# Kernel optimization log

Hardware: AMD Instinct MI355X
Metric: run time of the kernel (lower is better)

## Reference

```python
import jax, jax.numpy as jnp
import numpy as np

B, S, HID = 1, 2048, 2048
H, KV, D = 16, 4, 128  # head_dim = HID // H; GQA group size g = H // KV
THETA = 10000.0


def setup_inputs() -> dict:
    key = jax.random.key(0)
    ks = jax.random.split(key, 5)
    s = 0.02  # initializer_range
    return {
        "hidden_states": jax.random.normal(ks[0], (B, S, HID), jnp.float32),
        "wq": jax.random.normal(ks[1], (HID, H * D), jnp.float32) * s,
        "wk": jax.random.normal(ks[2], (HID, KV * D), jnp.float32) * s,
        "wv": jax.random.normal(ks[3], (HID, KV * D), jnp.float32) * s,
        "wo": jax.random.normal(ks[4], (H * D, HID), jnp.float32) * s,
        "attention_mask": jnp.ones((B, S), jnp.int32),
        "position_ids": jnp.broadcast_to(jnp.arange(S, dtype=jnp.int32), (B, S)),
    }


def _rope(x, position_ids):
    # x: [b, s, h, d]; rotate consecutive (even, odd) pairs by angle t * theta^{-2j/d}
    half = D // 2
    inv_freq = 1.0 / (THETA ** (jnp.arange(0, D, 2, dtype=jnp.float32) / D))  # [half]
    ang = position_ids[..., None].astype(jnp.float32) * inv_freq  # [b, s, half]
    cos = jnp.cos(ang)[:, :, None, :]  # [b, s, 1, half]
    sin = jnp.sin(ang)[:, :, None, :]
    xr = x.astype(jnp.float32).reshape(*x.shape[:-1], half, 2)
    x0, x1 = xr[..., 0], xr[..., 1]
    out = jnp.stack((x0 * cos - x1 * sin, x0 * sin + x1 * cos), axis=-1)
    return out.reshape(x.shape)


def reference(hidden_states, wq, wk, wv, wo, attention_mask, position_ids):
    b, s, _ = hidden_states.shape
    g = H // KV
    xq = (hidden_states @ wq).reshape(b, s, H, D)
    xk = (hidden_states @ wk).reshape(b, s, KV, D)
    xv = (hidden_states @ wv).reshape(b, s, KV, D)
    # GQA: each kv head repeated g consecutive times -> H heads (matches einops '(h g)')
    xk = jnp.repeat(xk, g, axis=2)
    xv = jnp.repeat(xv, g, axis=2)
    xq = _rope(xq, position_ids)
    xk = _rope(xk, position_ids)
    # causal + padding mask -> additive bias (0 or -inf), softmax in fp32
    causal = jnp.tril(jnp.ones((s, s), dtype=bool))[None, None]  # [1,1,q,k]
    mask = causal & (attention_mask[:, None, None, :] > 0)  # [b,1,q,k]
    scores = jnp.einsum('bqhd,bkhd->bhqk', xq.astype(jnp.float32), xk.astype(jnp.float32))
    scores = scores / jnp.sqrt(jnp.float32(D))
    scores = jnp.where(mask, scores, jnp.finfo(jnp.float32).min)
    attn_weights = jax.nn.softmax(scores, axis=-1)  # [b,h,q,k] fp32
    attn = jnp.einsum('bhqk,bkhd->bqhd', attn_weights, xv.astype(jnp.float32))
    return (attn.reshape(b, s, H * D).astype(hidden_states.dtype)) @ wo
```

## Files before the change

### kernel.cpp

```cpp
#include <hip/hip_runtime.h>
#include <hip/hip_bf16.h>

#define S_LEN 2048
#define HIDDIM 2048
#define NH 16
#define NKV 4
#define HD 128
#define KVROW 1024
#define QKVN 3072

typedef __attribute__((ext_vector_type(8))) short short8;
typedef __attribute__((ext_vector_type(8))) unsigned short ushort8;
typedef __attribute__((ext_vector_type(4))) unsigned short ushort4v;
typedef __attribute__((ext_vector_type(4))) float f32x4;

__device__ __forceinline__ unsigned short f2bf(float f) {
  union { float f; unsigned int u; } v; v.f = f;
  unsigned int r = (v.u + 0x7FFFu + ((v.u >> 16) & 1u)) >> 16;
  return (unsigned short)r;
}
__device__ __forceinline__ float bf2f(unsigned short h) {
  union { unsigned int u; float f; } v; v.u = ((unsigned int)h) << 16;
  return v.f;
}

__device__ __forceinline__ void gl2lds16(const unsigned short* src,
                                         unsigned short* dst) {
  __builtin_amdgcn_global_load_lds(
      (const __attribute__((address_space(1))) unsigned int*)src,
      (__attribute__((address_space(3))) unsigned int*)dst, 16, 0, 0);
}

__global__ __launch_bounds__(256) void h2b_kernel(const float* __restrict__ H,
                                                  unsigned short* __restrict__ Hb) {
  int i = (blockIdx.x * 256 + threadIdx.x) * 8;
  float4 a = *(const float4*)(H + i), b = *(const float4*)(H + i + 4);
  ushort8 r;
  r[0] = f2bf(a.x); r[1] = f2bf(a.y); r[2] = f2bf(a.z); r[3] = f2bf(a.w);
  r[4] = f2bf(b.x); r[5] = f2bf(b.y); r[6] = f2bf(b.z); r[7] = f2bf(b.w);
  *(ushort8*)(Hb + i) = r;
}

__global__ __launch_bounds__(256) void transpose_w(
    const float* __restrict__ W, unsigned short* __restrict__ Wt,
    int Nsrc, int Kdst, int n_off) {
  __shared__ unsigned short Ts[64][72];
  const int n0 = blockIdx.x * 64, k0 = blockIdx.y * 64;
  const int tid = threadIdx.x;
  const int c2 = (tid & 31) * 2, rb = tid >> 5;
#pragma unroll
  for (int p = 0; p < 8; ++p) {
    int r = rb + p * 8;
    float2 v = *(const float2*)&W[(size_t)(k0 + r) * Nsrc + n0 + c2];
    Ts[c2][r] = f2bf(v.x);
    Ts[c2 + 1][r] = f2bf(v.y);
  }
  __syncthreads();
  const int n = tid >> 2, kq = (tid & 3) * 16;
  ushort8 w0 = *(const ushort8*)&Ts[n][kq];
  ushort8 w1 = *(const ushort8*)&Ts[n][kq + 8];
  size_t base = (size_t)(n_off + n0 + n) * Kdst + k0 + kq;
  *(ushort8*)&Wt[base] = w0;
  *(ushort8*)&Wt[base + 8] = w1;
}

__global__ __launch_bounds__(256) void transpose_v(
    const unsigned short* __restrict__ KVb, unsigned short* __restrict__ Vt) {
  __shared__ unsigned short Ts[64][72];
  const int c0 = blockIdx.x * 64, s0 = blockIdx.y * 64;
  const int tid = threadIdx.x;
  const int sr = tid >> 2, cq = (tid & 3) * 16;
  ushort8 a = *(const ushort8*)&KVb[(size_t)(s0 + sr) * KVROW + 512 + c0 + cq];
  ushort8 b = *(const ushort8*)&KVb[(size_t)(s0 + sr) * KVROW + 512 + c0 + cq + 8];
#pragma unroll
  for (int j = 0; j < 8; ++j) { Ts[cq + j][sr] = a[j]; Ts[cq + 8 + j][sr] = b[j]; }
  __syncthreads();
  const int c = tid >> 2, sq = (tid & 3) * 16;
  ushort8 w0 = *(const ushort8*)&Ts[c][sq];
  ushort8 w1 = *(const ushort8*)&Ts[c][sq + 8];
  *(ushort8*)&Vt[(size_t)(c0 + c) * S_LEN + s0 + sq] = w0;
  *(ushort8*)&Vt[(size_t)(c0 + c) * S_LEN + s0 + sq + 8] = w1;
}

template <bool CF>
__global__ __launch_bounds__(256) void gemm_tn(
    const unsigned short* __restrict__ A, const unsigned short* __restrict__ Bt,
    void* __restrict__ C1, void* __restrict__ C2,
    int M, int N, int K, int splitcol, int ld1, int ld2) {
  __shared__ unsigned short As[128][72];
  __shared__ unsigned short Bs[64][72];
  const int m0 = blockIdx.y * 128, n0 = blockIdx.x * 64;
  const int tid = threadIdx.x, wid = tid >> 6, lane = tid & 63;
  const int wr = wid >> 1, wc = wid & 1;
  const int lr = lane & 15, lg = lane >> 4;

  f32x4 acc[4][2];
#pragma unroll
  for (int m = 0; m < 4; ++m)
#pragma unroll
    for (int n = 0; n < 2; ++n) acc[m][n] = (f32x4){0.f, 0.f, 0.f, 0.f};

  const int ar = tid >> 1, ac = (tid & 1) * 32;
  const int br = tid >> 2, bc = (tid & 3) * 16;

  ushort8 areg[4], breg[2];
  auto loadA = [&](int k0) {
#pragma unroll
    for (int i = 0; i < 4; ++i)
      areg[i] = *(const ushort8*)(A + (size_t)(m0 + ar) * K + k0 + ac + i * 8);
  };
  auto loadB = [&](int k0) {
    breg[0] = *(const ushort8*)(Bt + (size_t)(n0 + br) * K + k0 + bc);
    breg[1] = *(const ushort8*)(Bt + (size_t)(n0 + br) * K + k0 + bc + 8);
  };
  auto writeS = [&]() {
#pragma unroll
    for (int i = 0; i < 4; ++i) *(ushort8*)&As[ar][ac + i * 8] = areg[i];
    *(ushort8*)&Bs[br][bc] = breg[0];
    *(ushort8*)&Bs[br][bc + 8] = breg[1];
  };

  loadA(0); loadB(0);
  writeS();

  for (int k0 = 0; k0 < K; k0 += 64) {
    __syncthreads();
    if (k0 + 64 < K) {
      loadA(k0 + 64); loadB(k0 + 64);
      asm volatile("" ::: "memory");
    }
#pragma unroll
    for (int s = 0; s < 2; ++s) {
      short8 af[4], bfv[2];
#pragma unroll
      for (int m = 0; m < 4; ++m)
        af[m] = *(const short8*)&As[wr * 64 + m * 16 + lr][s * 32 + lg * 8];
#pragma unroll
      for (int n = 0; n < 2; ++n)
        bfv[n] = *(const short8*)&Bs[wc * 32 + n * 16 + lr][s * 32 + lg * 8];
#pragma unroll
      for (int m = 0; m < 4; ++m)
#pragma unroll
        for (int n = 0; n < 2; ++n)
          acc[m][n] = __builtin_amdgcn_mfma_f32_16x16x32_bf16(af[m], bfv[n], acc[m][n], 0, 0, 0);
    }
    __syncthreads();
    if (k0 + 64 < K) writeS();
  }

#pragma unroll
  for (int m = 0; m < 4; ++m)
#pragma unroll
    for (int n = 0; n < 2; ++n)
#pragma unroll
      for (int r = 0; r < 4; ++r) {
        int row = m0 + wr * 64 + m * 16 + lg * 4 + r;
        int col = n0 + wc * 32 + n * 16 + lr;
        float v = acc[m][n][r];
        if (CF) ((float*)C1)[(size_t)row * ld1 + col] = v;
        else if (col < splitcol) ((unsigned short*)C1)[(size_t)row * ld1 + col] = f2bf(v);
        else ((unsigned short*)C2)[(size_t)row * ld2 + (col - splitcol)] = f2bf(v);
      }
}

__global__ void rope2(unsigned short* __restrict__ Q,
                      unsigned short* __restrict__ KV,
                      const int* __restrict__ pos) {
  int idx = blockIdx.x * blockDim.x + threadIdx.x;
  if (idx >= S_LEN * 64) return;
  int s = idx >> 6, j = idx & 63;
  float inv = exp2f(-0.2076205059304703f * (float)j);
  float ang = (float)pos[s] * inv;
  float sn, cs;
  __sincosf(ang, &sn, &cs);
  auto rot = [&](unsigned short* base) {
    unsigned* p = (unsigned*)base;
    unsigned v = *p;
    float x0 = bf2f((unsigned short)(v & 0xffff));
    float x1 = bf2f((unsigned short)(v >> 16));
    unsigned r = (unsigned)f2bf(x0 * cs - x1 * sn) |
                 ((unsigned)f2bf(x0 * sn + x1 * cs) << 16);
    *p = r;
  };
#pragma unroll
  for (int hh = 0; hh < NH; ++hh) rot(Q + (size_t)s * HIDDIM + hh * HD + 2 * j);
#pragma unroll
  for (int hh = 0; hh < NKV; ++hh) rot(KV + (size_t)s * KVROW + hh * HD + 2 * j);
}

__global__ void maskbits_kernel(const int* __restrict__ amask,
                                unsigned* __restrict__ mb) {
  int w = threadIdx.x;
  unsigned m = 0;
#pragma unroll
  for (int b = 0; b < 32; ++b) m |= (amask[w * 32 + b] != 0 ? 1u : 0u) << b;
  mb[w] = m;
}

__global__ __launch_bounds__(512) void attn_kernel(
    const unsigned short* __restrict__ Qb, const unsigned short* __restrict__ KVb,
    const unsigned short* __restrict__ VtG, const unsigned* __restrict__ mbits,
    unsigned short* __restrict__ Ob,
    unsigned short* __restrict__ Opart, float* __restrict__ Lpart, int nsplit) {
  const int x = (int)blockIdx.x;
  const int qt = 63 - (x >> 2);
  const int c = x & 3;
  const int kvh = (int)blockIdx.y;
  const int nch = (qt >> 4) + 1;
  if (nsplit == 0) { if (c != 0) return; }
  else if (c >= nch) return;
  const int qb = qt * 32;
  int kbeg = 0, kend = qb + 32;
  bool partial = false;
  if (nsplit && nch > 1) {
    kbeg = c * 512;
    kend = min(kend, kbeg + 512);
    partial = true;
  }

  __shared__ unsigned short Klds[2][32 * 128];
  __shared__ unsigned short Vlds[2][128 * 32];
  __shared__ unsigned short Plds[8][16][40];
  const int tid = threadIdx.x, wid = tid >> 6, lane = tid & 63;
  const int lr = lane & 15, lg = lane >> 4;
  const int h = kvh * 4 + (wid & 3);
  const int rg = wid >> 2;
  const int qrow0 = qb + rg * 16;

  short8 qf[4];
  {
    const unsigned short* qp = Qb + (size_t)(qrow0 + lr) * HIDDIM + h * HD;
#pragma unroll
    for (int cc = 0; cc < 4; ++cc) qf[cc] = *(const short8*)(qp + cc * 32 + lg * 8);
  }
  f32x4 o[8];
#pragma unroll
  for (int cc = 0; cc < 8; ++cc) o[cc] = (f32x4){0.f, 0.f, 0.f, 0.f};
  float lsum = 0.f;

  const unsigned short* Vg = VtG + (size_t)(kvh * HD) * S_LEN;

  const int ksrow = (wid << 2) + (lane >> 4);
  const int kssrc = ((lane & 15) << 4) ^ ((ksrow & 7) << 4);
  const int vsd = (wid << 4) + (lane >> 2);
  const int vssrc = (((lane & 3) << 4) ^ ((vsd & 3) << 4));

  auto stage = [&](int kt, int b) {
    gl2lds16(KVb + (size_t)(kt + ksrow) * KVROW + kvh * HD + (kssrc >> 1),
             &Klds[b][0] + (size_t)wid * 512);
    gl2lds16(Vg + (size_t)vsd * S_LEN + kt + (vssrc >> 1),
             &Vlds[b][0] + (size_t)wid * 512);
  };

  stage(kbeg, 0);

  const int qr = qrow0 + lr;
  const float SCALE = 0.08838834764831845f;
  int cur = 0;

  for (int kt = kbeg; kt < kend; kt += 32) {
    __syncthreads();
    if (kt + 32 < kend) stage(kt + 32, cur ^ 1);

    f32x4 sc[2];
    sc[0] = (f32x4){0.f, 0.f, 0.f, 0.f};
    sc[1] = (f32x4){0.f, 0.f, 0.f, 0.f};
    const unsigned short* kbase = &Klds[cur][0];
    __builtin_amdgcn_s_setprio(1);
#pragma unroll
    for (int t = 0; t < 2; ++t)
#pragma unroll
      for (int cc = 0; cc < 4; ++cc) {
        short8 kf = *(const short8*)(kbase + ((t * 16 + lr) << 7) +
                                     ((((cc << 6) + (lg << 4)) ^ ((lr & 7) << 4)) >> 1));
        sc[t] = __builtin_amdgcn_mfma_f32_16x16x32_bf16(kf, qf[cc], sc[t], 0, 0, 0);
      }
    __builtin_amdgcn_s_setprio(0);
    const unsigned mw = mbits[kt >> 5];
    float p[2][4];
#pragma unroll
    for (int t = 0; t < 2; ++t)
#pragma unroll
      for (int r = 0; r < 4; ++r) {
        int kk = t * 16 + lg * 4 + r;
        bool ok = (kt + kk <= qr) && ((mw >> kk) & 1u);
        float s = ok ? sc[t][r] * SCALE - 3.0f : -1e30f;
        float pv = __expf(s);
        p[t][r] = pv;
        lsum += pv;
      }
#pragma unroll
    for (int t = 0; t < 2; ++t) {
      ushort4v pk;
#pragma unroll
      for (int r = 0; r < 4; ++r) pk[r] = f2bf(p[t][r]);
      *(ushort4v*)&Plds[wid][lr][t * 16 + lg * 4] = pk;
    }
    short8 pf = *(const short8*)&Plds[wid][lr][lg * 8];
    const unsigned short* vbase = &Vlds[cur][0];
    __builtin_amdgcn_s_setprio(1);
#pragma unroll
    for (int cc = 0; cc < 8; ++cc) {
      short8 vf = *(const short8*)(vbase + ((cc * 16 + lr) << 5) +
                                   ((lg ^ (lr & 3)) << 3));
      o[cc] = __builtin_amdgcn_mfma_f32_16x16x32_bf16(pf, vf, o[cc], 0, 0, 0);
    }
    __builtin_amdgcn_s_setprio(0);
    cur ^= 1;
  }

  float ls = lsum;
  ls += __shfl_xor(ls, 16, 64);
  ls += __shfl_xor(ls, 32, 64);

  if (!partial) {
    float lrec[4];
#pragma unroll
    for (int r = 0; r < 4; ++r) lrec[r] = 1.0f / __shfl(ls, lg * 4 + r, 16);
#pragma unroll
    for (int cc = 0; cc < 8; ++cc)
#pragma unroll
      for (int r = 0; r < 4; ++r) {
        const int row = qrow0 + lg * 4 + r;
        Ob[(size_t)row * HIDDIM + h * HD + cc * 16 + lr] = f2bf(o[cc][r] * lrec[r]);
      }
  } else {
    const int g = qt >> 4, j = qt & 15;
    const int base = (g == 1) ? 0 : (g == 2) ? 32 : 80;
    const int slot = base + j * nch + c + 144 * kvh;
    if (lg == 0) Lpart[slot * 128 + (wid & 3) * 32 + rg * 16 + lr] = ls;
#pragma unroll
    for (int cc = 0; cc < 8; ++cc)
#pragma unroll
      for (int r = 0; r < 4; ++r)
        Opart[(size_t)slot * 16384 + (wid & 3) * 4096 +
              (rg * 16 + lg * 4 + r) * 128 + cc * 16 + lr] = f2bf(o[cc][r]);
  }
}

__global__ __launch_bounds__(256) void combine_kernel(
    const unsigned short* __restrict__ Opart, const float* __restrict__ Lpart,
    unsigned short* __restrict__ Ab) {
  const int qt = 16 + (int)blockIdx.x;
  const int kvh = (int)blockIdx.y;
  const int nch = (qt >> 4) + 1;
  const int g = qt >> 4, j = qt & 15;
  const int base = (g == 1) ? 0 : (g == 2) ? 32 : 80;
  const int s0 = base + j * nch + 144 * kvh;
  const int tid = threadIdx.x;
  const int rowid = tid >> 1;
  const int d0 = (tid & 1) * 64;
  float L = 0.f;
  for (int cc = 0; cc < nch; ++cc) L += Lpart[(s0 + cc) * 128 + rowid];
  const float linv = 1.0f / L;
  const int h = kvh * 4 + (rowid >> 5);
  const int row = qt * 32 + (rowid & 31);
  unsigned short* dst = Ab + (size_t)row * HIDDIM + h * HD + d0;
  for (int i = 0; i < 64; i += 8) {
    float acc[8] = {0, 0, 0, 0, 0, 0, 0, 0};
    for (int cc = 0; cc < nch; ++cc) {
      ushort8 v = *(const ushort8*)&Opart[(size_t)(s0 + cc) * 16384 +
                                          rowid * 128 + d0 + i];
#pragma unroll
      for (int k = 0; k < 8; ++k) acc[k] += bf2f(v[k]);
    }
    ushort8 r;
#pragma unroll
    for (int k = 0; k < 8; ++k) r[k] = f2bf(acc[k] * linv);
    *(ushort8*)(dst + i) = r;
  }
}

extern "C" void kernel_launch(void* const* d_in, const int* in_sizes, int n_in,
                              void* d_out, int out_size, void* d_ws, size_t ws_size,
                              hipStream_t stream) {
  const float* hidden = (const float*)d_in[0];
  const float* wq = (const float*)d_in[1];
  const float* wk = (const float*)d_in[2];
  const float* wv = (const float*)d_in[3];
  const float* wo = (const float*)d_in[4];
  const int* amask = (const int*)d_in[5];
  const int* pos = (const int*)d_in[6];

  unsigned short* Qb = (unsigned short*)d_ws;
  unsigned short* KVb = Qb + (size_t)S_LEN * HIDDIM;
  unsigned short* Ab = KVb + (size_t)S_LEN * KVROW;
  unsigned short* WT1 = Ab + (size_t)S_LEN * HIDDIM;
  unsigned short* Hb = WT1 + (size_t)QKVN * HIDDIM;
  float* out = (float*)d_out;

  unsigned short* Opart = WT1;
  unsigned short* Vt_chunk = WT1 + (size_t)576 * 16384;
  unsigned* mbits_chunk = (unsigned*)((char*)d_ws + 41943040ull);
  float* Lpart = (float*)((char*)d_ws + 41943296ull);
  const size_t need_chunk = 42238208ull;
  unsigned short* Vt_fb = WT1 + (size_t)HIDDIM * HIDDIM;
  unsigned* mbits_fb = (unsigned*)((char*)d_ws + 31457280ull);

  const int nsplit = (ws_size >= need_chunk) ? 1 : 0;
  unsigned short* Vt = nsplit ? Vt_chunk : Vt_fb;
  unsigned* mbits = nsplit ? mbits_chunk : mbits_fb;

  dim3 blk(256);
  h2b_kernel<<<2048, blk, 0, stream>>>(hidden, Hb);
  transpose_w<<<dim3(32, 32), blk, 0, stream>>>(wq, WT1, HIDDIM, HIDDIM, 0);
  transpose_w<<<dim3(8, 32), blk, 0, stream>>>(wk, WT1, 512, HIDDIM, 2048);
  transpose_w<<<dim3(8, 32), blk, 0, stream>>>(wv, WT1, 512, HIDDIM, 2560);
  gemm_tn<false><<<dim3(QKVN / 64, S_LEN / 128), blk, 0, stream>>>(
      Hb, WT1, Qb, KVb, S_LEN, QKVN, HIDDIM, 2048, HIDDIM, KVROW);
  transpose_v<<<dim3(8, 32), blk, 0, stream>>>(KVb, Vt);
  rope2<<<(S_LEN * 64 + 255) / 256, blk, 0, stream>>>(Qb, KVb, pos);
  maskbits_kernel<<<1, 64, 0, stream>>>(amask, mbits);
  attn_kernel<<<dim3(256, NKV), dim3(512), 0, stream>>>(
      Qb, KVb, Vt, mbits, Ab, Opart, Lpart, nsplit);
  if (nsplit)
    combine_kernel<<<dim3(48, NKV), blk, 0, stream>>>(Opart, Lpart, Ab);
  transpose_w<<<dim3(32, 32), blk, 0, stream>>>(wo, WT1, HIDDIM, HIDDIM, 0);
  gemm_tn<true><<<dim3(HIDDIM / 64, S_LEN / 128), blk, 0, stream>>>(
      Ab, WT1, out, nullptr, S_LEN, HIDDIM, HIDDIM, HIDDIM, HIDDIM, 0);
}
```

Before: 184.6 us.

## Stage GEMM tiles via direct global-to-LDS loads with double buffering and XOR swizzle

Replaces the register-staged global→LDS copy in gemm_tn with direct global-to-LDS 16-byte loads (gl2lds16) into double-buffered shared tiles. The padded layout is replaced by an XOR swizzle on 16-byte chunks to avoid LDS bank conflicts. The second barrier per k-step is removed. The aim is to cut VGPR pressure and load/store instruction overhead and to overlap the next tile's fetch with the MFMAs. It doubles LDS use and relies on the async load completing before the single barrier, with no explicit vmcnt wait shown.

```diff
diff --git a/kernel.cpp b/kernel.cpp
--- a/kernel.cpp
+++ b/kernel.cpp
@@ -87,8 +87,8 @@
     const unsigned short* __restrict__ A, const unsigned short* __restrict__ Bt,
     void* __restrict__ C1, void* __restrict__ C2,
     int M, int N, int K, int splitcol, int ld1, int ld2) {
-  __shared__ unsigned short As[128][72];
-  __shared__ unsigned short Bs[64][72];
+  __shared__ unsigned short As[2][128 * 64];
+  __shared__ unsigned short Bs[2][64 * 64];
   const int m0 = blockIdx.y * 128, n0 = blockIdx.x * 64;
   const int tid = threadIdx.x, wid = tid >> 6, lane = tid & 63;
   const int wr = wid >> 1, wc = wid & 1;
@@ -100,52 +100,52 @@
 #pragma unroll
     for (int n = 0; n < 2; ++n) acc[m][n] = (f32x4){0.f, 0.f, 0.f, 0.f};
 
-  const int ar = tid >> 1, ac = (tid & 1) * 32;
-  const int br = tid >> 2, bc = (tid & 3) * 16;
-
-  ushort8 areg[4], breg[2];
-  auto loadA = [&](int k0) {
-#pragma unroll
-    for (int i = 0; i < 4; ++i)
-      areg[i] = *(const ushort8*)(A + (size_t)(m0 + ar) * K + k0 + ac + i * 8);
+  const int srow = lane >> 3;
+  const int scolb = (lane & 7) << 4;
+  auto stage = [&](int k0, int b) {
+#pragma unroll
+    for (int j = 0; j < 4; ++j) {
+      int row = wid * 32 + j * 8 + srow;
+      int src = (scolb ^ ((row & 7) << 4)) >> 1;
+      gl2lds16(A + (size_t)(m0 + row) * K + k0 + src,
+               &As[b][(wid * 32 + j * 8) * 64]);
+    }
+#pragma unroll
+    for (int j = 0; j < 2; ++j) {
+      int row = wid * 16 + j * 8 + srow;
+      int src = (scolb ^ ((row & 7) << 4)) >> 1;
+      gl2lds16(Bt + (size_t)(n0 + row) * K + k0 + src,
+               &Bs[b][(wid * 16 + j * 8) * 64]);
+    }
   };
-  auto loadB = [&](int k0) {
-    breg[0] = *(const ushort8*)(Bt + (size_t)(n0 + br) * K + k0 + bc);
-    breg[1] = *(const ushort8*)(Bt + (size_t)(n0 + br) * K + k0 + bc + 8);
-  };
-  auto writeS = [&]() {
-#pragma unroll
-    for (int i = 0; i < 4; ++i) *(ushort8*)&As[ar][ac + i * 8] = areg[i];
-    *(ushort8*)&Bs[br][bc] = breg[0];
-    *(ushort8*)&Bs[br][bc + 8] = breg[1];
-  };
-
-  loadA(0); loadB(0);
-  writeS();
-
+
+  stage(0, 0);
+  int cur = 0;
   for (int k0 = 0; k0 < K; k0 += 64) {
     __syncthreads();
-    if (k0 + 64 < K) {
-      loadA(k0 + 64); loadB(k0 + 64);
-      asm volatile("" ::: "memory");
-    }
+    if (k0 + 64 < K) stage(k0 + 64, cur ^ 1);
 #pragma unroll
     for (int s = 0; s < 2; ++s) {
       short8 af[4], bfv[2];
 #pragma unroll
-      for (int m = 0; m < 4; ++m)
-        af[m] = *(const short8*)&As[wr * 64 + m * 16 + lr][s * 32 + lg * 8];
-#pragma unroll
-      for (int n = 0; n < 2; ++n)
-        bfv[n] = *(const short8*)&Bs[wc * 32 + n * 16 + lr][s * 32 + lg * 8];
+      for (int m = 0; m < 4; ++m) {
+        int row = wr * 64 + m * 16 + lr;
+        int off = ((s * 64 + lg * 16) ^ ((row & 7) << 4)) >> 1;
+        af[m] = *(const short8*)&As[cur][row * 64 + off];
+      }
+#pragma unroll
+      for (int n = 0; n < 2; ++n) {
+        int row = wc * 32 + n * 16 + lr;
+        int off = ((s * 64 + lg * 16) ^ ((row & 7) << 4)) >> 1;
+        bfv[n] = *(const short8*)&Bs[cur][row * 64 + off];
+      }
 #pragma unroll
       for (int m = 0; m < 4; ++m)
 #pragma unroll
         for (int n = 0; n < 2; ++n)
           acc[m][n] = __builtin_amdgcn_mfma_f32_16x16x32_bf16(af[m], bfv[n], acc[m][n], 0, 0, 0);
     }
-    __syncthreads();
-    if (k0 + 64 < K) writeS();
+    cur ^= 1;
   }
 
 #pragma unroll
```

After: 171.4 us. 7.1% less time.
